# Kernel optimization log

Hardware: AMD Instinct MI355X
Metric: run time of the kernel (lower is better)

## Reference

```python
import jax, jax.numpy as jnp
import numpy as np

B, H, C, PX, PY = 2, 16, 4, 16, 16
EXTRA = 64
HD = 64
N = C * PX * PY + EXTRA


def setup_inputs() -> dict:
    key = jax.random.key(0)
    ks = jax.random.split(key, 8)
    q = jax.random.normal(ks[0], (B, H, N, HD), jnp.float32)
    k = jax.random.normal(ks[1], (B, H, N, HD), jnp.float32)
    v = jax.random.normal(ks[2], (B, H, N, HD), jnp.float32)
    # valid SE(3) world-to-camera matrices: rotation via QR (det fixed to +1)
    A = jax.random.normal(ks[3], (B, C, 3, 3), jnp.float32)
    Q, _ = jnp.linalg.qr(A)
    det = jnp.linalg.det(Q)
    Q = Q * det[..., None, None]
    t = 0.5 * jax.random.normal(ks[4], (B, C, 3), jnp.float32)
    top = jnp.concatenate([Q, t[..., None]], -1)
    bot = jnp.broadcast_to(jnp.array([0.0, 0.0, 0.0, 1.0], jnp.float32), (B, C, 1, 4))
    viewmats = jnp.concatenate([top, bot], -2)
    # pinhole intrinsics (no skew)
    fx = 300.0 + 10.0 * jax.random.uniform(ks[5], (B, C))
    fy = 300.0 + 10.0 * jax.random.uniform(ks[6], (B, C))
    z = jnp.zeros((B, C)); o = jnp.ones((B, C))
    cx = 128.0 * o; cy = 128.0 * o
    Ks = jnp.stack([jnp.stack([fx, z, cx], -1), jnp.stack([z, fy, cy], -1), jnp.stack([z, z, o], -1)], -2)
    spatial_mask = jnp.arange(N) >= EXTRA  # first EXTRA tokens are non-spatial
    return {"q": q, "k": k, "v": v, "viewmats": viewmats, "Ks": Ks,
            "spatial_mask": spatial_mask, "patches_x": PX, "patches_y": PY,
            "image_width": 256, "image_height": 256}


def _invert_SE3(T):
    R = T[..., :3, :3]; t = T[..., :3, 3]
    Rinv = jnp.swapaxes(R, -1, -2)
    tinv = -jnp.einsum('...ij,...j->...i', Rinv, t)
    top = jnp.concatenate([Rinv, tinv[..., None]], -1)
    bot = jnp.broadcast_to(jnp.array([0.0, 0.0, 0.0, 1.0], T.dtype), T.shape[:-2] + (1, 4))
    return jnp.concatenate([top, bot], -2)


def _lift(K3):
    out = jnp.zeros(K3.shape[:-2] + (4, 4), K3.dtype)
    return out.at[..., :3, :3].set(K3).at[..., 3, 3].set(1.0)


def _invert_K(K):
    fx = K[..., 0, 0]; fy = K[..., 1, 1]; cx = K[..., 0, 2]; cy = K[..., 1, 2]
    z = jnp.zeros_like(fx); o = jnp.ones_like(fx)
    return jnp.stack([jnp.stack([1.0 / fx, z, -cx / fx], -1),
                      jnp.stack([z, 1.0 / fy, -cy / fy], -1),
                      jnp.stack([z, z, o], -1)], -2)


def _transform(feats, M, cosx, sinx, cosy, siny, inverse):
    # Block-diagonal: [tiled 4x4 projmat on D/2 | RoPE-x on D/4 | RoPE-y on D/4]
    Bq, Hq, Nq, D = feats.shape
    h2 = D // 2; h4 = D // 4
    p = feats[..., :h2].reshape(Bq, Hq, Nq, h2 // 4, 4)
    p = jnp.einsum('bnij,bhnkj->bhnki', M, p).reshape(Bq, Hq, Nq, h2)

    def rope(x, c, s):
        c = c[None, None]; s = s[None, None]  # [1,1,N,nf]
        xa, xb = x[..., : x.shape[-1] // 2], x[..., x.shape[-1] // 2:]
        if inverse:
            return jnp.concatenate([c * xa - s * xb, s * xa + c * xb], -1)
        return jnp.concatenate([c * xa + s * xb, -s * xa + c * xb], -1)

    rx = rope(feats[..., h2:h2 + h4], cosx, sinx)
    ry = rope(feats[..., h2 + h4:], cosy, siny)
    return jnp.concatenate([p, rx, ry], -1)


def reference(q, k, v, viewmats, Ks, spatial_mask, patches_x, patches_y, image_width, image_height):
    D = q.shape[-1]
    Bq, Cq = viewmats.shape[:2]
    # normalized intrinsics
    fx = Ks[..., 0, 0] / image_width; fy = Ks[..., 1, 1] / image_height
    cx = Ks[..., 0, 2] / image_width - 0.5; cy = Ks[..., 1, 2] / image_height - 0.5
    z = jnp.zeros_like(fx); o = jnp.ones_like(fx)
    Kn = jnp.stack([jnp.stack([fx, z, cx], -1), jnp.stack([z, fy, cy], -1), jnp.stack([z, z, o], -1)], -2)
    P = jnp.einsum('...ij,...jk->...ik', _lift(Kn), viewmats)          # [B,C,4,4]
    P_T = jnp.swapaxes(P, -1, -2)
    P_inv = jnp.einsum('...ij,...jk->...ik', _invert_SE3(viewmats), _lift(_invert_K(Kn)))
    # RoPE tables over spatial tokens (split convention, base=100, scale=1)
    nf = D // 8
    freqs = 100.0 ** (-jnp.arange(nf, dtype=jnp.float32) / nf)
    pos_x = jnp.tile(jnp.arange(patches_x, dtype=jnp.float32), patches_y * Cq)
    pos_y = jnp.tile(jnp.repeat(jnp.arange(patches_y, dtype=jnp.float32), patches_x), Cq)
    ang_x = pos_x[:, None] * freqs; ang_y = pos_y[:, None] * freqs  # [S,nf]
    mask = spatial_mask
    S = pos_x.shape[0]
    # index of each token within the spatial-token ordering (masked scatter, vectorized)
    sidx = jnp.clip(jnp.cumsum(mask.astype(jnp.int32)) - 1, 0, S - 1)
    m = mask[:, None]
    cosx = jnp.where(m, jnp.cos(ang_x)[sidx], 1.0); sinx = jnp.where(m, jnp.sin(ang_x)[sidx], 0.0)
    cosy = jnp.where(m, jnp.cos(ang_y)[sidx], 1.0); siny = jnp.where(m, jnp.sin(ang_y)[sidx], 0.0)
    cam = sidx // (patches_x * patches_y)  # camera id per token
    I4 = jnp.eye(4, dtype=q.dtype)
    mm = mask[None, :, None, None]
    Mq = jnp.where(mm, P_T[:, cam], I4)    # [B,N,4,4]
    Mkv = jnp.where(mm, P_inv[:, cam], I4)
    Mo = jnp.where(mm, P[:, cam], I4)
    qt = _transform(q, Mq, cosx, sinx, cosy, siny, False)
    kt = _transform(k, Mkv, cosx, sinx, cosy, siny, False)
    vt = _transform(v, Mkv, cosx, sinx, cosy, siny, False)
    logits = jnp.einsum('bhqd,bhkd->bhqk', qt, kt) / jnp.sqrt(jnp.float32(D))
    attn = jax.nn.softmax(logits, axis=-1)
    out = jnp.einsum('bhqk,bhkd->bhqd', attn, vt)
    return _transform(out, Mo, cosx, sinx, cosy, siny, True)
```

## Files before the change

### kernel.cpp

```cpp
#include <hip/hip_runtime.h>
#include <math.h>

typedef _Float16 f16;
typedef _Float16 f16x8 __attribute__((ext_vector_type(8)));
typedef __fp16 h16x2 __attribute__((ext_vector_type(2)));
typedef float f32x16 __attribute__((ext_vector_type(16)));
typedef unsigned int u32;
typedef u32 u32x4 __attribute__((ext_vector_type(4)));

constexpr int Bc = 2, Hc = 16, Cc = 4, PXc = 16, PYc = 16, EXTRAc = 64, HDc = 64;
constexpr int Nc = Cc * PXc * PYc + EXTRAc;
constexpr int BH = Bc * Hc;
constexpr int KT = 64;
constexpr int NKT = Nc / KT;
constexpr int KS = 4;
constexpr int NSPLIT = 16;
constexpr int NQT = Nc / 32;
constexpr int NBLK = NQT * BH * KS;

constexpr size_t TENS_SZ  = (size_t)BH * Nc * HDc * 2;
constexpr size_t PBH      = (size_t)Nc * 128;
constexpr size_t QF_OFF   = 0;
constexpr size_t KF_OFF   = QF_OFF + TENS_SZ;
constexpr size_t VT_OFF   = KF_OFF + TENS_SZ;
constexpr size_t PART_OFF = VT_OFF + TENS_SZ;
constexpr size_t ML_OFF   = PART_OFF + (size_t)KS * TENS_SZ;

__device__ const float FREQS[8] = {1.0f, 0.5623413252f, 0.31622776601f, 0.17782794100f,
                                   0.1f, 0.05623413252f, 0.031622776602f, 0.017782794100f};
constexpr float QSCALE = 0.125f * 1.4426950408889634f;

__device__ __forceinline__ void compute_M(float* M, const float* __restrict__ vm,
                                          const float* __restrict__ Ks3, int b, int cam, int which) {
    const float* V  = vm + (b * Cc + cam) * 16;
    const float* K3 = Ks3 + (b * Cc + cam) * 9;
    float fx = K3[0] * (1.0f / 256.0f);
    float fy = K3[4] * (1.0f / 256.0f);
    float cx = K3[2] * (1.0f / 256.0f) - 0.5f;
    float cy = K3[5] * (1.0f / 256.0f) - 0.5f;
    if (which == 2) {
        float IV[16];
        IV[0] = V[0]; IV[1] = V[4]; IV[2] = V[8];
        IV[4] = V[1]; IV[5] = V[5]; IV[6] = V[9];
        IV[8] = V[2]; IV[9] = V[6]; IV[10] = V[10];
        float tx = V[3], ty = V[7], tz = V[11];
        IV[3]  = -(IV[0] * tx + IV[1] * ty + IV[2] * tz);
        IV[7]  = -(IV[4] * tx + IV[5] * ty + IV[6] * tz);
        IV[11] = -(IV[8] * tx + IV[9] * ty + IV[10] * tz);
        IV[12] = 0.f; IV[13] = 0.f; IV[14] = 0.f; IV[15] = 1.f;
        float ifx = 1.f / fx, ify = 1.f / fy;
        float ncx = -cx * ifx, ncy = -cy * ify;
        #pragma unroll
        for (int i = 0; i < 4; ++i) {
            M[i * 4 + 0] = IV[i * 4 + 0] * ifx;
            M[i * 4 + 1] = IV[i * 4 + 1] * ify;
            M[i * 4 + 2] = IV[i * 4 + 0] * ncx + IV[i * 4 + 1] * ncy + IV[i * 4 + 2];
            M[i * 4 + 3] = IV[i * 4 + 3];
        }
    } else {
        float P[16];
        #pragma unroll
        for (int j = 0; j < 4; ++j) {
            P[0 * 4 + j] = fx * V[0 * 4 + j] + cx * V[2 * 4 + j];
            P[1 * 4 + j] = fy * V[1 * 4 + j] + cy * V[2 * 4 + j];
            P[2 * 4 + j] = V[2 * 4 + j];
            P[3 * 4 + j] = V[3 * 4 + j];
        }
        if (which == 0) {
            #pragma unroll
            for (int i = 0; i < 16; ++i) M[i] = P[i];
        } else {
            #pragma unroll
            for (int i = 0; i < 4; ++i)
                #pragma unroll
                for (int j = 0; j < 4; ++j) M[i * 4 + j] = P[j * 4 + i];
        }
    }
}

template <bool INV>
__device__ __forceinline__ void xf_seg(float* v16, int seg, int n, int b, int which,
                                       const float* __restrict__ vm, const float* __restrict__ Ks3) {
    if (n < EXTRAc) return;
    int sidx = n - EXTRAc;
    int cam = sidx >> 8;
    if (seg < 2) {
        float M[16];
        compute_M(M, vm, Ks3, b, cam, which);
        #pragma unroll
        for (int g = 0; g < 4; ++g) {
            float a0 = v16[4 * g], a1 = v16[4 * g + 1], a2 = v16[4 * g + 2], a3 = v16[4 * g + 3];
            v16[4 * g + 0] = M[0]  * a0 + M[1]  * a1 + M[2]  * a2 + M[3]  * a3;
            v16[4 * g + 1] = M[4]  * a0 + M[5]  * a1 + M[6]  * a2 + M[7]  * a3;
            v16[4 * g + 2] = M[8]  * a0 + M[9]  * a1 + M[10] * a2 + M[11] * a3;
            v16[4 * g + 3] = M[12] * a0 + M[13] * a1 + M[14] * a2 + M[15] * a3;
        }
    } else {
        float pos = (seg == 2) ? (float)(sidx & (PXc - 1)) : (float)((sidx >> 4) & (PYc - 1));
        #pragma unroll
        for (int f = 0; f < 8; ++f) {
            float s, c;
            __sincosf(pos * FREQS[f], &s, &c);
            float xa = v16[f], xb = v16[8 + f];
            if (INV) {
                v16[f]     = c * xa - s * xb;
                v16[8 + f] = s * xa + c * xb;
            } else {
                v16[f]     = c * xa + s * xb;
                v16[8 + f] = -s * xa + c * xb;
            }
        }
    }
}

__device__ __forceinline__ u32 pkh(float a, float b) {
    h16x2 r = __builtin_amdgcn_cvt_pkrtz(a, b);
    return __builtin_bit_cast(u32, r);
}

__device__ __forceinline__ f32x16 zero16() {
    f32x16 z = {0.f,0.f,0.f,0.f,0.f,0.f,0.f,0.f,0.f,0.f,0.f,0.f,0.f,0.f,0.f,0.f};
    return z;
}

__global__ void prope_xform_kernel(const float* __restrict__ q, const float* __restrict__ k,
                                   const float* __restrict__ v,
                                   const float* __restrict__ viewmats, const float* __restrict__ Ks,
                                   char* __restrict__ wsb) {
    __shared__ f16 tile[64][72];
    if (blockIdx.x < 1088) {
        int id = blockIdx.x * 256 + threadIdx.x;
        int seg = id & 3;
        int rid = id >> 2;
        int tensor = rid / (BH * Nc);
        int row = rid - tensor * (BH * Nc);
        int n = row % Nc;
        int bhq = row / Nc;
        int b = bhq >> 4;
        const float* src = (tensor ? k : q) + (size_t)row * 64 + seg * 16;
        float vals[16];
        #pragma unroll
        for (int i = 0; i < 4; ++i) ((float4*)vals)[i] = ((const float4*)src)[i];
        xf_seg<false>(vals, seg, n, b, tensor ? 2 : 1, viewmats, Ks);
        float scale = tensor ? 1.0f : QSCALE;
        f16 o[16];
        #pragma unroll
        for (int i = 0; i < 16; ++i) o[i] = (f16)(vals[i] * scale);
        if (tensor == 0) {
            char* base = wsb + QF_OFF + (size_t)bhq * PBH + (size_t)(n >> 5) * 4096;
            int qq = n & 31;
            *(float4*)(base + (seg * 2 + 0) * 512 + qq * 16) = ((float4*)o)[0];
            *(float4*)(base + (seg * 2 + 1) * 512 + qq * 16) = ((float4*)o)[1];
        } else {
            char* base = wsb + KF_OFF + (size_t)bhq * PBH + (size_t)(n >> 6) * 8192;
            int kk = n & 63, rh = kk >> 5, qq = kk & 31;
            *(float4*)(base + (((seg * 2 + rh) * 2 + 0) * 32 + qq) * 16) = ((float4*)o)[0];
            *(float4*)(base + (((seg * 2 + rh) * 2 + 1) * 32 + qq) * 16) = ((float4*)o)[1];
        }
    } else {
        int vb = blockIdx.x - 1088;
        int kt = vb >> 5, bh = vb & 31;
        int b = bh >> 4;
        int t = threadIdx.x;
        {
            int r = t >> 2, seg = t & 3;
            int n = kt * 64 + r;
            const float* src = v + ((size_t)bh * Nc + n) * 64 + seg * 16;
            float vals[16];
            #pragma unroll
            for (int i = 0; i < 4; ++i) ((float4*)vals)[i] = ((const float4*)src)[i];
            xf_seg<false>(vals, seg, n, b, 2, viewmats, Ks);
            #pragma unroll
            for (int i = 0; i < 16; ++i) tile[r][seg * 16 + i] = (f16)vals[i];
        }
        __syncthreads();
        {
            int d = t >> 2, ks = t & 3;
            f16 o[16];
            #pragma unroll
            for (int j = 0; j < 16; ++j) o[j] = tile[ks * 16 + j][d];
            int dh = d >> 5, dq = d & 31;
            char* base = wsb + VT_OFF + (size_t)bh * PBH + (size_t)kt * 8192;
            *(float4*)(base + (((ks * 2 + dh) * 2 + 0) * 32 + dq) * 16) = ((float4*)o)[0];
            *(float4*)(base + (((ks * 2 + dh) * 2 + 1) * 32 + dq) * 16) = ((float4*)o)[1];
        }
    }
}

__device__ __forceinline__ void tile_step(
    const char* kb, const char* vb, const f16x8 (&qb)[4], int lane, int h,
    f32x16& o0, f32x16& o1, float& mrun, float& lrun)
{
    f16x8 ka0[4], ka1[4], va0[4], va1[4];
    #pragma unroll
    for (int c = 0; c < 4; ++c) {
        ka0[c] = *(const f16x8*)(kb + (c * 2 + 0) * 1024 + lane * 16);
        ka1[c] = *(const f16x8*)(kb + (c * 2 + 1) * 1024 + lane * 16);
        va0[c] = *(const f16x8*)(vb + (c * 2 + 0) * 1024 + lane * 16);
        va1[c] = *(const f16x8*)(vb + (c * 2 + 1) * 1024 + lane * 16);
    }

    f32x16 s0 = zero16(), s1 = zero16();
    __builtin_amdgcn_s_setprio(1);
    #pragma unroll
    for (int c = 0; c < 4; ++c) {
        s0 = __builtin_amdgcn_mfma_f32_32x32x16_f16(ka0[c], qb[c], s0, 0, 0, 0);
        s1 = __builtin_amdgcn_mfma_f32_32x32x16_f16(ka1[c], qb[c], s1, 0, 0, 0);
    }
    __builtin_amdgcn_s_setprio(0);

    float q8[8];
    #pragma unroll
    for (int i = 0; i < 4; ++i) {
        q8[i]     = fmaxf(fmaxf(s0[4*i], s0[4*i+1]), fmaxf(s0[4*i+2], s0[4*i+3]));
        q8[4 + i] = fmaxf(fmaxf(s1[4*i], s1[4*i+1]), fmaxf(s1[4*i+2], s1[4*i+3]));
    }
    float tm = fmaxf(fmaxf(fmaxf(q8[0], q8[1]), fmaxf(q8[2], q8[3])),
                     fmaxf(fmaxf(q8[4], q8[5]), fmaxf(q8[6], q8[7])));
    tm = fmaxf(tm, __shfl_xor(tm, 32, 64));
    if (!__all(tm <= mrun + 8.0f)) {
        float nm = fmaxf(mrun, tm);
        float corr = exp2f(mrun - nm);
        mrun = nm;
        lrun *= corr;
        #pragma unroll
        for (int i = 0; i < 16; ++i) { o0[i] *= corr; o1[i] *= corr; }
    }
    #pragma unroll
    for (int i = 0; i < 16; ++i) s0[i] = exp2f(s0[i] - mrun);
    #pragma unroll
    for (int i = 0; i < 16; ++i) s1[i] = exp2f(s1[i] - mrun);
    float a8[8];
    #pragma unroll
    for (int i = 0; i < 4; ++i) {
        a8[i]     = (s0[4*i] + s0[4*i+1]) + (s0[4*i+2] + s0[4*i+3]);
        a8[4 + i] = (s1[4*i] + s1[4*i+1]) + (s1[4*i+2] + s1[4*i+3]);
    }
    float ps = ((a8[0] + a8[1]) + (a8[2] + a8[3])) + ((a8[4] + a8[5]) + (a8[6] + a8[7]));
    ps += __shfl_xor(ps, 32, 64);
    lrun += ps;

    u32 U0[8], U1[8];
    #pragma unroll
    for (int g = 0; g < 4; ++g) {
        U0[g * 2 + 0] = pkh(s0[4 * g + 0], s0[4 * g + 1]);
        U0[g * 2 + 1] = pkh(s0[4 * g + 2], s0[4 * g + 3]);
        U1[g * 2 + 0] = pkh(s1[4 * g + 0], s1[4 * g + 1]);
        U1[g * 2 + 1] = pkh(s1[4 * g + 2], s1[4 * g + 3]);
    }

    u32 pw[4][4];
    #pragma unroll
    for (int c = 0; c < 4; ++c) {
        const u32* Us = (c < 2) ? U0 : U1;
        int gl = 2 * (c & 1);
        u32 x0 = Us[(gl + 1) * 2 + 0], x1 = Us[(gl + 1) * 2 + 1];
        u32 y0 = Us[gl * 2 + 0],       y1 = Us[gl * 2 + 1];
        u32 s0w = h ? y0 : x0;
        u32 s1w = h ? y1 : x1;
        u32 r0 = (u32)__shfl_xor((int)s0w, 32, 64);
        u32 r1 = (u32)__shfl_xor((int)s1w, 32, 64);
        u32 own0 = h ? x0 : y0, own1 = h ? x1 : y1;
        pw[c][0] = h ? r0 : own0;
        pw[c][1] = h ? r1 : own1;
        pw[c][2] = h ? own0 : r0;
        pw[c][3] = h ? own1 : r1;
    }

    __builtin_amdgcn_s_setprio(1);
    #pragma unroll
    for (int c = 0; c < 4; ++c) {
        u32x4 fw = {pw[c][0], pw[c][1], pw[c][2], pw[c][3]};
        f16x8 pb = __builtin_bit_cast(f16x8, fw);
        o0 = __builtin_amdgcn_mfma_f32_32x32x16_f16(va0[c], pb, o0, 0, 0, 0);
        o1 = __builtin_amdgcn_mfma_f32_32x32x16_f16(va1[c], pb, o1, 0, 0, 0);
    }
    __builtin_amdgcn_s_setprio(0);
}

__global__ __launch_bounds__(256, 2) void prope_attn_mfma_kernel(
    const char* __restrict__ wsb, char* __restrict__ partO, float* __restrict__ partML) {
    __shared__ float os[4][32][64];
    __shared__ float mls[4][2][32];

    const int tid = threadIdx.x;
    const int wv = tid >> 6, lane = tid & 63;
    const int q = lane & 31, h = lane >> 5;
    const int bid = blockIdx.x;
    const int ll = (bid & 7) * (NBLK / 8) + (bid >> 3);
    const int qt = ll % NQT;
    const int rest = ll / NQT;
    const int bh = rest & 31, z = rest >> 5;
    const int g = z * 4 + wv;
    const int ts = (NKT * g) / NSPLIT, te = (NKT * (g + 1)) / NSPLIT;

    const char* kfb = wsb + KF_OFF + (size_t)bh * PBH;
    const char* vfb = wsb + VT_OFF + (size_t)bh * PBH;
    const char* qfb = wsb + QF_OFF + (size_t)bh * PBH + (size_t)qt * 4096;

    f16x8 qb[4];
    #pragma unroll
    for (int c = 0; c < 4; ++c) qb[c] = *(const f16x8*)(qfb + c * 1024 + lane * 16);

    f32x16 o0 = zero16(), o1 = zero16();
    float mrun = -1e30f, lrun = 0.f;

    for (int it = ts; it < te; ++it)
        tile_step(kfb + (size_t)it * 8192, vfb + (size_t)it * 8192,
                  qb, lane, h, o0, o1, mrun, lrun);

    #pragma unroll
    for (int i = 0; i < 16; ++i) {
        os[wv][i][lane]      = o0[i];
        os[wv][16 + i][lane] = o1[i];
    }
    if (h == 0) { mls[wv][0][q] = mrun; mls[wv][1][q] = lrun; }
    __syncthreads();

    if (wv == 0) {
        float m4[4], l4[4];
        #pragma unroll
        for (int w = 0; w < 4; ++w) { m4[w] = mls[w][0][q]; l4[w] = mls[w][1][q]; }
        float mB = fmaxf(fmaxf(m4[0], m4[1]), fmaxf(m4[2], m4[3]));
        float u4[4], lB = 0.f;
        #pragma unroll
        for (int w = 0; w < 4; ++w) { u4[w] = exp2f(m4[w] - mB); lB += u4[w] * l4[w]; }
        float inv = 1.f / lB;
        f32x16 a0 = zero16(), a1 = zero16();
        #pragma unroll
        for (int w = 0; w < 4; ++w) {
            #pragma unroll
            for (int i = 0; i < 16; ++i) {
                a0[i] += u4[w] * os[w][i][lane];
                a1[i] += u4[w] * os[w][16 + i][lane];
            }
        }
        char* ob = (char*)os;
        #pragma unroll
        for (int gg = 0; gg < 4; ++gg) {
            #pragma unroll
            for (int w = 0; w < 2; ++w) {
                u32 u0 = pkh(a0[4 * gg + 2 * w] * inv, a0[4 * gg + 2 * w + 1] * inv);
                u32 u1 = pkh(a1[4 * gg + 2 * w] * inv, a1[4 * gg + 2 * w + 1] * inv);
                int col0 = 16 * gg + 8 * h + 4 * w;
                *(u32*)(ob + ((q * 128 + col0) ^ ((q & 7) << 4))) = u0;
                *(u32*)(ob + ((q * 128 + col0 + 64) ^ ((q & 7) << 4))) = u1;
            }
        }
        if (h == 0) {
            float2 mlv = {mB, lB};
            ((float2*)partML)[((size_t)z * BH + bh) * Nc + qt * 32 + q] = mlv;
        }
        {
            int rr = lane >> 1, half = lane & 1;
            char* dst = partO + (((size_t)z * BH + bh) * Nc + qt * 32 + rr) * 128 + half * 64;
            #pragma unroll
            for (int j = 0; j < 4; ++j) {
                float4 val = *(float4*)(ob + ((rr * 128 + half * 64 + j * 16) ^ ((rr & 7) << 4)));
                ((float4*)dst)[j] = val;
            }
        }
    }
}

__global__ void prope_combine_kernel(const char* __restrict__ wsb,
                                     const float* __restrict__ viewmats, const float* __restrict__ Ks,
                                     float* __restrict__ out) {
    int id = blockIdx.x * 256 + threadIdx.x;
    int seg = id & 3, rid = id >> 2;
    int n = rid % Nc, bh = rid / Nc, b = bh >> 4;
    const float2* ml = (const float2*)(wsb + ML_OFF);
    float m[KS], l[KS];
    float mstar = -1e30f;
    #pragma unroll
    for (int s = 0; s < KS; ++s) {
        float2 v = ml[((size_t)s * BH + bh) * Nc + n];
        m[s] = v.x; l[s] = v.y;
        mstar = fmaxf(mstar, m[s]);
    }
    float wsum = 0.f, wgt[KS];
    #pragma unroll
    for (int s = 0; s < KS; ++s) { wgt[s] = exp2f(m[s] - mstar) * l[s]; wsum += wgt[s]; }
    float inv = 1.f / wsum;
    float acc[16];
    #pragma unroll
    for (int i = 0; i < 16; ++i) acc[i] = 0.f;
    #pragma unroll
    for (int s = 0; s < KS; ++s) {
        const char* op = wsb + PART_OFF + (((size_t)s * BH + bh) * Nc + n) * 128 + seg * 32;
        f16x8 a0 = *(const f16x8*)op;
        f16x8 a1 = *(const f16x8*)(op + 16);
        #pragma unroll
        for (int i = 0; i < 8; ++i) acc[i] += wgt[s] * (float)a0[i];
        #pragma unroll
        for (int i = 0; i < 8; ++i) acc[8 + i] += wgt[s] * (float)a1[i];
    }
    #pragma unroll
    for (int i = 0; i < 16; ++i) acc[i] *= inv;
    xf_seg<true>(acc, seg, n, b, 0, viewmats, Ks);
    float* go = out + ((size_t)bh * Nc + n) * 64 + seg * 16;
    #pragma unroll
    for (int i = 0; i < 4; ++i) ((float4*)go)[i] = ((const float4*)acc)[i];
}

extern "C" void kernel_launch(void* const* d_in, const int* in_sizes, int n_in,
                              void* d_out, int out_size, void* d_ws, size_t ws_size,
                              hipStream_t stream) {
    const float* q        = (const float*)d_in[0];
    const float* k        = (const float*)d_in[1];
    const float* v        = (const float*)d_in[2];
    const float* viewmats = (const float*)d_in[3];
    const float* Ks       = (const float*)d_in[4];
    char* wsb  = (char*)d_ws;
    float* out = (float*)d_out;

    prope_xform_kernel<<<1088 + 544, 256, 0, stream>>>(q, k, v, viewmats, Ks, wsb);
    prope_attn_mfma_kernel<<<NBLK, 256, 0, stream>>>(wsb, wsb + PART_OFF,
                                                     (float*)(wsb + ML_OFF));
    prope_combine_kernel<<<(BH * Nc * 4) / 256, 256, 0, stream>>>(wsb, viewmats, Ks, out);
}
```

Baseline: 56.68 us.

## Share double-buffered K/V tiles in LDS across four query-tile waves

The attention kernel is reorganised so that each block's four waves each own a different 32-row query tile and walk the same key range. Before, the waves split the key range for a single query tile and their results were merged in LDS. K/V tiles are now loaded once per block into double-buffered LDS with global_load_lds and read by all four waves, which cuts global K/V traffic and removes the intra-block softmax merge. The costs are a __syncthreads per key tile, idle waves in the last query block (34 tiles over 9 blocks of 4), and fewer blocks overall. The s_setprio hints are dropped.

```diff
diff --git a/kernel.cpp b/kernel.cpp
--- a/kernel.cpp
+++ b/kernel.cpp
@@ -14,9 +14,8 @@
 constexpr int KT = 64;
 constexpr int NKT = Nc / KT;
 constexpr int KS = 4;
-constexpr int NSPLIT = 16;
-constexpr int NQT = Nc / 32;
-constexpr int NBLK = NQT * BH * KS;
+constexpr int NQB = 9;
+constexpr int NBLK = NQB * BH * KS;
 
 constexpr size_t TENS_SZ  = (size_t)BH * Nc * HDc * 2;
 constexpr size_t PBH      = (size_t)Nc * 128;
@@ -118,6 +117,11 @@
     return __builtin_bit_cast(u32, r);
 }
 
+__device__ __forceinline__ void gld16(const void* g, void* l) {
+    __builtin_amdgcn_global_load_lds((const __attribute__((address_space(1))) unsigned int*)g,
+                                     (__attribute__((address_space(3))) unsigned int*)l, 16, 0, 0);
+}
+
 __device__ __forceinline__ f32x16 zero16() {
     f32x16 z = {0.f,0.f,0.f,0.f,0.f,0.f,0.f,0.f,0.f,0.f,0.f,0.f,0.f,0.f,0.f,0.f};
     return z;
@@ -187,173 +191,159 @@
     }
 }
 
-__device__ __forceinline__ void tile_step(
-    const char* kb, const char* vb, const f16x8 (&qb)[4], int lane, int h,
-    f32x16& o0, f32x16& o1, float& mrun, float& lrun)
-{
-    f16x8 ka0[4], ka1[4], va0[4], va1[4];
-    #pragma unroll
-    for (int c = 0; c < 4; ++c) {
-        ka0[c] = *(const f16x8*)(kb + (c * 2 + 0) * 1024 + lane * 16);
-        ka1[c] = *(const f16x8*)(kb + (c * 2 + 1) * 1024 + lane * 16);
-        va0[c] = *(const f16x8*)(vb + (c * 2 + 0) * 1024 + lane * 16);
-        va1[c] = *(const f16x8*)(vb + (c * 2 + 1) * 1024 + lane * 16);
-    }
-
-    f32x16 s0 = zero16(), s1 = zero16();
-    __builtin_amdgcn_s_setprio(1);
-    #pragma unroll
-    for (int c = 0; c < 4; ++c) {
-        s0 = __builtin_amdgcn_mfma_f32_32x32x16_f16(ka0[c], qb[c], s0, 0, 0, 0);
-        s1 = __builtin_amdgcn_mfma_f32_32x32x16_f16(ka1[c], qb[c], s1, 0, 0, 0);
-    }
-    __builtin_amdgcn_s_setprio(0);
-
-    float q8[8];
-    #pragma unroll
-    for (int i = 0; i < 4; ++i) {
-        q8[i]     = fmaxf(fmaxf(s0[4*i], s0[4*i+1]), fmaxf(s0[4*i+2], s0[4*i+3]));
-        q8[4 + i] = fmaxf(fmaxf(s1[4*i], s1[4*i+1]), fmaxf(s1[4*i+2], s1[4*i+3]));
-    }
-    float tm = fmaxf(fmaxf(fmaxf(q8[0], q8[1]), fmaxf(q8[2], q8[3])),
-                     fmaxf(fmaxf(q8[4], q8[5]), fmaxf(q8[6], q8[7])));
-    tm = fmaxf(tm, __shfl_xor(tm, 32, 64));
-    if (!__all(tm <= mrun + 8.0f)) {
-        float nm = fmaxf(mrun, tm);
-        float corr = exp2f(mrun - nm);
-        mrun = nm;
-        lrun *= corr;
-        #pragma unroll
-        for (int i = 0; i < 16; ++i) { o0[i] *= corr; o1[i] *= corr; }
-    }
-    #pragma unroll
-    for (int i = 0; i < 16; ++i) s0[i] = exp2f(s0[i] - mrun);
-    #pragma unroll
-    for (int i = 0; i < 16; ++i) s1[i] = exp2f(s1[i] - mrun);
-    float a8[8];
-    #pragma unroll
-    for (int i = 0; i < 4; ++i) {
-        a8[i]     = (s0[4*i] + s0[4*i+1]) + (s0[4*i+2] + s0[4*i+3]);
-        a8[4 + i] = (s1[4*i] + s1[4*i+1]) + (s1[4*i+2] + s1[4*i+3]);
-    }
-    float ps = ((a8[0] + a8[1]) + (a8[2] + a8[3])) + ((a8[4] + a8[5]) + (a8[6] + a8[7]));
-    ps += __shfl_xor(ps, 32, 64);
-    lrun += ps;
-
-    u32 U0[8], U1[8];
-    #pragma unroll
-    for (int g = 0; g < 4; ++g) {
-        U0[g * 2 + 0] = pkh(s0[4 * g + 0], s0[4 * g + 1]);
-        U0[g * 2 + 1] = pkh(s0[4 * g + 2], s0[4 * g + 3]);
-        U1[g * 2 + 0] = pkh(s1[4 * g + 0], s1[4 * g + 1]);
-        U1[g * 2 + 1] = pkh(s1[4 * g + 2], s1[4 * g + 3]);
-    }
-
-    u32 pw[4][4];
-    #pragma unroll
-    for (int c = 0; c < 4; ++c) {
-        const u32* Us = (c < 2) ? U0 : U1;
-        int gl = 2 * (c & 1);
-        u32 x0 = Us[(gl + 1) * 2 + 0], x1 = Us[(gl + 1) * 2 + 1];
-        u32 y0 = Us[gl * 2 + 0],       y1 = Us[gl * 2 + 1];
-        u32 s0w = h ? y0 : x0;
-        u32 s1w = h ? y1 : x1;
-        u32 r0 = (u32)__shfl_xor((int)s0w, 32, 64);
-        u32 r1 = (u32)__shfl_xor((int)s1w, 32, 64);
-        u32 own0 = h ? x0 : y0, own1 = h ? x1 : y1;
-        pw[c][0] = h ? r0 : own0;
-        pw[c][1] = h ? r1 : own1;
-        pw[c][2] = h ? own0 : r0;
-        pw[c][3] = h ? own1 : r1;
-    }
-
-    __builtin_amdgcn_s_setprio(1);
-    #pragma unroll
-    for (int c = 0; c < 4; ++c) {
-        u32x4 fw = {pw[c][0], pw[c][1], pw[c][2], pw[c][3]};
-        f16x8 pb = __builtin_bit_cast(f16x8, fw);
-        o0 = __builtin_amdgcn_mfma_f32_32x32x16_f16(va0[c], pb, o0, 0, 0, 0);
-        o1 = __builtin_amdgcn_mfma_f32_32x32x16_f16(va1[c], pb, o1, 0, 0, 0);
-    }
-    __builtin_amdgcn_s_setprio(0);
-}
-
 __global__ __launch_bounds__(256, 2) void prope_attn_mfma_kernel(
     const char* __restrict__ wsb, char* __restrict__ partO, float* __restrict__ partML) {
-    __shared__ float os[4][32][64];
-    __shared__ float mls[4][2][32];
+    __shared__ char smem[32768];
 
     const int tid = threadIdx.x;
     const int wv = tid >> 6, lane = tid & 63;
     const int q = lane & 31, h = lane >> 5;
     const int bid = blockIdx.x;
-    const int ll = (bid & 7) * (NBLK / 8) + (bid >> 3);
-    const int qt = ll % NQT;
-    const int rest = ll / NQT;
+    const int l = (bid & 7) * (NBLK / 8) + (bid >> 3);
+    const int qblk = l % NQB;
+    const int rest = l / NQB;
     const int bh = rest & 31, z = rest >> 5;
-    const int g = z * 4 + wv;
-    const int ts = (NKT * g) / NSPLIT, te = (NKT * (g + 1)) / NSPLIT;
+    const int ts = (NKT * z) / KS, te = (NKT * (z + 1)) / KS;
+    const int qtile = qblk * 4 + wv;
+    const bool act = qtile < 34;
 
     const char* kfb = wsb + KF_OFF + (size_t)bh * PBH;
     const char* vfb = wsb + VT_OFF + (size_t)bh * PBH;
-    const char* qfb = wsb + QF_OFF + (size_t)bh * PBH + (size_t)qt * 4096;
+
+    auto stage = [&](int bsel, int t) {
+        char* dst = smem + bsel * 16384 + wv * 1024;
+        const char* ksrc = kfb + (size_t)t * 8192 + wv * 1024 + lane * 16;
+        const char* vsrc = vfb + (size_t)t * 8192 + wv * 1024 + lane * 16;
+        gld16(ksrc,        dst);
+        gld16(ksrc + 4096, dst + 4096);
+        gld16(vsrc,        dst + 8192);
+        gld16(vsrc + 4096, dst + 12288);
+    };
+
+    stage(0, ts);
 
     f16x8 qb[4];
-    #pragma unroll
-    for (int c = 0; c < 4; ++c) qb[c] = *(const f16x8*)(qfb + c * 1024 + lane * 16);
+    if (act) {
+        const char* qfb = wsb + QF_OFF + (size_t)bh * PBH + (size_t)qtile * 4096;
+        #pragma unroll
+        for (int c = 0; c < 4; ++c) qb[c] = *(const f16x8*)(qfb + c * 1024 + lane * 16);
+    }
 
     f32x16 o0 = zero16(), o1 = zero16();
-    float mrun = -1e30f, lrun = 0.f;
-
-    for (int it = ts; it < te; ++it)
-        tile_step(kfb + (size_t)it * 8192, vfb + (size_t)it * 8192,
-                  qb, lane, h, o0, o1, mrun, lrun);
-
-    #pragma unroll
-    for (int i = 0; i < 16; ++i) {
-        os[wv][i][lane]      = o0[i];
-        os[wv][16 + i][lane] = o1[i];
-    }
-    if (h == 0) { mls[wv][0][q] = mrun; mls[wv][1][q] = lrun; }
+    float mrun = -1e30f, lloc = 0.f;
+
+    int cur = 0;
+    for (int it = ts; it < te; ++it) {
+        __syncthreads();
+        if (it + 1 < te) stage(cur ^ 1, it + 1);
+        if (act) {
+            const char* kb = smem + cur * 16384;
+            const char* vb = kb + 8192;
+            f16x8 ka0[4], ka1[4], va0[4], va1[4];
+            #pragma unroll
+            for (int c = 0; c < 4; ++c) {
+                ka0[c] = *(const f16x8*)(kb + (c * 2 + 0) * 1024 + lane * 16);
+                ka1[c] = *(const f16x8*)(kb + (c * 2 + 1) * 1024 + lane * 16);
+                va0[c] = *(const f16x8*)(vb + (c * 2 + 0) * 1024 + lane * 16);
+                va1[c] = *(const f16x8*)(vb + (c * 2 + 1) * 1024 + lane * 16);
+            }
+
+            f32x16 s0 = zero16(), s1 = zero16();
+            #pragma unroll
+            for (int c = 0; c < 4; ++c) {
+                s0 = __builtin_amdgcn_mfma_f32_32x32x16_f16(ka0[c], qb[c], s0, 0, 0, 0);
+                s1 = __builtin_amdgcn_mfma_f32_32x32x16_f16(ka1[c], qb[c], s1, 0, 0, 0);
+            }
+
+            float q8[8];
+            #pragma unroll
+            for (int i = 0; i < 4; ++i) {
+                q8[i]     = fmaxf(fmaxf(s0[4*i], s0[4*i+1]), fmaxf(s0[4*i+2], s0[4*i+3]));
+                q8[4 + i] = fmaxf(fmaxf(s1[4*i], s1[4*i+1]), fmaxf(s1[4*i+2], s1[4*i+3]));
+            }
+            float tm = fmaxf(fmaxf(fmaxf(q8[0], q8[1]), fmaxf(q8[2], q8[3])),
+                             fmaxf(fmaxf(q8[4], q8[5]), fmaxf(q8[6], q8[7])));
+            tm = fmaxf(tm, __shfl_xor(tm, 32, 64));
+            if (!__all(tm <= mrun + 8.0f)) {
+                float nm = fmaxf(mrun, tm);
+                float corr = exp2f(mrun - nm);
+                mrun = nm;
+                lloc *= corr;
+                #pragma unroll
+                for (int i = 0; i < 16; ++i) { o0[i] *= corr; o1[i] *= corr; }
+            }
+            #pragma unroll
+            for (int i = 0; i < 16; ++i) s0[i] = exp2f(s0[i] - mrun);
+            #pragma unroll
+            for (int i = 0; i < 16; ++i) s1[i] = exp2f(s1[i] - mrun);
+            float a8[8];
+            #pragma unroll
+            for (int i = 0; i < 4; ++i) {
+                a8[i]     = (s0[4*i] + s0[4*i+1]) + (s0[4*i+2] + s0[4*i+3]);
+                a8[4 + i] = (s1[4*i] + s1[4*i+1]) + (s1[4*i+2] + s1[4*i+3]);
+            }
+            lloc += ((a8[0] + a8[1]) + (a8[2] + a8[3])) + ((a8[4] + a8[5]) + (a8[6] + a8[7]));
+
+            u32 U0[8], U1[8];
+            #pragma unroll
+            for (int g = 0; g < 4; ++g) {
+                U0[g * 2 + 0] = pkh(s0[4 * g + 0], s0[4 * g + 1]);
+                U0[g * 2 + 1] = pkh(s0[4 * g + 2], s0[4 * g + 3]);
+                U1[g * 2 + 0] = pkh(s1[4 * g + 0], s1[4 * g + 1]);
+                U1[g * 2 + 1] = pkh(s1[4 * g + 2], s1[4 * g + 3]);
+            }
+
+            u32 pw[4][4];
+            #pragma unroll
+            for (int c = 0; c < 4; ++c) {
+                const u32* Us = (c < 2) ? U0 : U1;
+                int gl = 2 * (c & 1);
+                u32 x0 = Us[(gl + 1) * 2 + 0], x1 = Us[(gl + 1) * 2 + 1];
+                u32 y0 = Us[gl * 2 + 0],       y1 = Us[gl * 2 + 1];
+                u32 s0w = h ? y0 : x0;
+                u32 s1w = h ? y1 : x1;
+                u32 r0 = (u32)__shfl_xor((int)s0w, 32, 64);
+                u32 r1 = (u32)__shfl_xor((int)s1w, 32, 64);
+                u32 own0 = h ? x0 : y0, own1 = h ? x1 : y1;
+                pw[c][0] = h ? r0 : own0;
+                pw[c][1] = h ? r1 : own1;
+                pw[c][2] = h ? own0 : r0;
+                pw[c][3] = h ? own1 : r1;
+            }
+            #pragma unroll
+            for (int c = 0; c < 4; ++c) {
+                u32x4 fw = {pw[c][0], pw[c][1], pw[c][2], pw[c][3]};
+                f16x8 pb = __builtin_bit_cast(f16x8, fw);
+                o0 = __builtin_amdgcn_mfma_f32_32x32x16_f16(va0[c], pb, o0, 0, 0, 0);
+                o1 = __builtin_amdgcn_mfma_f32_32x32x16_f16(va1[c], pb, o1, 0, 0, 0);
+            }
+        }
+        cur ^= 1;
+    }
     __syncthreads();
 
-    if (wv == 0) {
-        float m4[4], l4[4];
-        #pragma unroll
-        for (int w = 0; w < 4; ++w) { m4[w] = mls[w][0][q]; l4[w] = mls[w][1][q]; }
-        float mB = fmaxf(fmaxf(m4[0], m4[1]), fmaxf(m4[2], m4[3]));
-        float u4[4], lB = 0.f;
-        #pragma unroll
-        for (int w = 0; w < 4; ++w) { u4[w] = exp2f(m4[w] - mB); lB += u4[w] * l4[w]; }
-        float inv = 1.f / lB;
-        f32x16 a0 = zero16(), a1 = zero16();
-        #pragma unroll
-        for (int w = 0; w < 4; ++w) {
-            #pragma unroll
-            for (int i = 0; i < 16; ++i) {
-                a0[i] += u4[w] * os[w][i][lane];
-                a1[i] += u4[w] * os[w][16 + i][lane];
-            }
-        }
-        char* ob = (char*)os;
-        #pragma unroll
-        for (int gg = 0; gg < 4; ++gg) {
+    if (act) {
+        float lrun = lloc + __shfl_xor(lloc, 32, 64);
+        float invl = 1.f / lrun;
+        char* ob = smem + wv * 4096;
+        #pragma unroll
+        for (int g = 0; g < 4; ++g) {
             #pragma unroll
             for (int w = 0; w < 2; ++w) {
-                u32 u0 = pkh(a0[4 * gg + 2 * w] * inv, a0[4 * gg + 2 * w + 1] * inv);
-                u32 u1 = pkh(a1[4 * gg + 2 * w] * inv, a1[4 * gg + 2 * w + 1] * inv);
-                int col0 = 16 * gg + 8 * h + 4 * w;
+                u32 u0 = pkh(o0[4 * g + 2 * w] * invl, o0[4 * g + 2 * w + 1] * invl);
+                u32 u1 = pkh(o1[4 * g + 2 * w] * invl, o1[4 * g + 2 * w + 1] * invl);
+                int col0 = 16 * g + 8 * h + 4 * w;
                 *(u32*)(ob + ((q * 128 + col0) ^ ((q & 7) << 4))) = u0;
                 *(u32*)(ob + ((q * 128 + col0 + 64) ^ ((q & 7) << 4))) = u1;
             }
         }
         if (h == 0) {
-            float2 mlv = {mB, lB};
-            ((float2*)partML)[((size_t)z * BH + bh) * Nc + qt * 32 + q] = mlv;
+            float2 mlv = {mrun, lrun};
+            ((float2*)partML)[((size_t)z * BH + bh) * Nc + qtile * 32 + q] = mlv;
         }
         {
             int rr = lane >> 1, half = lane & 1;
-            char* dst = partO + (((size_t)z * BH + bh) * Nc + qt * 32 + rr) * 128 + half * 64;
+            char* dst = partO + (((size_t)z * BH + bh) * Nc + qtile * 32 + rr) * 128 + half * 64;
             #pragma unroll
             for (int j = 0; j < 4; ++j) {
                 float4 val = *(float4*)(ob + ((rr * 128 + half * 64 + j * 16) ^ ((rr & 7) << 4)));
```

After: 48.59 us. 14.3% less time.
